# Performance work log

Hardware: AMD Instinct MI355X
Metric: run time of the kernel (lower is better)

The kernel has to match this reference:

```python
import jax, jax.numpy as jnp
import numpy as np

NH = 64
KS = 3
H_DIM = 32
IN_DIM = 1

# U-Net conv shapes, matching get_indices(unet_nh=64)
KERN_SHAPES = ([(NH, 2, KS, KS)] + [(NH, NH, KS, KS)] * 7
               + [(NH, 2 * NH, KS, KS), (NH, NH, KS, KS)] * 3
               + [(2, NH, 1, 1)])
BIAS_SHAPES = [(NH,)] * 14 + [(2,)]
KERN_SIZES = [int(np.prod(s)) for s in KERN_SHAPES]
BIAS_SIZES = [int(np.prod(s)) for s in BIAS_SHAPES]
OUT_DIM = sum(KERN_SIZES) + sum(BIAS_SIZES)  # 592002


def hypernet(hp, W1, b1, W2, b2, Wo, bo):
    # hp: [B, in_dim] -> per-sample flat weight vector [B, OUT_DIM]
    h = hp @ W1.T + b1          # no activation between lin1/lin2 (as in source)
    h = h @ W2.T + b2
    w = jnp.tanh(h @ Wo.T + bo)
    wl, bl = [], []
    off = 0
    for s, n in zip(KERN_SHAPES, KERN_SIZES):
        wl.append(w[:, off:off + n].reshape(-1, *s)); off += n
    for s, n in zip(BIAS_SHAPES, BIAS_SIZES):
        bl.append(w[:, off:off + n].reshape(-1, *s)); off += n
    return wl, bl, w


def bconv(x, w, b, pad):
    # per-sample conv: x [B,C,H,W], w [B,O,C,k,k], b [B,O]
    def one(xi, wi, bi):
        y = jax.lax.conv_general_dilated(xi[None], wi, (1, 1), [(pad, pad), (pad, pad)])
        return y[0] + bi[:, None, None]
    return jax.vmap(one)(x, w, b)


def maxpool2(x):
    B, C, H, W = x.shape
    return x.reshape(B, C, H // 2, 2, W // 2, 2).max(axis=(3, 5))


def up2_ac(x):
    # bilinear upsample scale=2, align_corners=True
    B, C, H, W = x.shape
    Ho, Wo = 2 * H, 2 * W
    ys = (jnp.arange(Ho, dtype=jnp.float32) * (H - 1) / (Ho - 1))
    y0 = jnp.floor(ys).astype(jnp.int32); y1 = jnp.minimum(y0 + 1, H - 1)
    wy = (ys - y0.astype(jnp.float32))[None, None, :, None]
    xs = (jnp.arange(Wo, dtype=jnp.float32) * (W - 1) / (Wo - 1))
    x0 = jnp.floor(xs).astype(jnp.int32); x1 = jnp.minimum(x0 + 1, W - 1)
    wx = (xs - x0.astype(jnp.float32))[None, None, None, :]
    r = x[:, :, y0, :] * (1 - wy) + x[:, :, y1, :] * wy
    return r[:, :, :, x0] * (1 - wx) + r[:, :, :, x1] * wx


def setup_inputs() -> dict:
    key = jax.random.key(0)
    ks = jax.random.split(key, 9)
    B, H, W = 8, 256, 256
    s1 = 1.0 / (IN_DIM * NH) ** 0.5
    s2 = 1.0 / (H_DIM * NH) ** 0.5
    return {
        "zf": jax.random.normal(ks[0], (B, H, W, 2), jnp.float32),
        "y": jax.random.normal(ks[1], (B, H, W, 2), jnp.float32),
        "hyperparams": jax.random.uniform(ks[2], (B, IN_DIM), jnp.float32),
        "W1": jax.random.normal(ks[3], (H_DIM, IN_DIM), jnp.float32) * s1,
        "b1": jax.random.normal(ks[4], (H_DIM,), jnp.float32) * s1,
        "W2": jax.random.normal(ks[5], (H_DIM, H_DIM), jnp.float32) * s2,
        "b2": jax.random.normal(ks[6], (H_DIM,), jnp.float32) * s2,
        "Wo": jax.random.normal(ks[7], (OUT_DIM, H_DIM), jnp.float32) * s2,
        "bo": jax.random.normal(ks[8], (OUT_DIM,), jnp.float32) * s2,
    }


def reference(zf, y, hyperparams, W1, b1, W2, b2, Wo, bo):
    wl, bl, flat = hypernet(hyperparams, W1, b1, W2, b2, Wo, bo)
    # l1 over all generated weights+biases == sum |flat| per sample
    l1_weights = jnp.sum(jnp.abs(flat), axis=1)
    relu = jax.nn.relu
    x = jnp.transpose(zf, (0, 3, 1, 2))  # [B,2,H,W]
    x = relu(bconv(x, wl[0], bl[0], 1))
    conv1 = relu(bconv(x, wl[1], bl[1], 1))
    x = maxpool2(conv1)
    x = relu(bconv(x, wl[2], bl[2], 1))
    conv2 = relu(bconv(x, wl[3], bl[3], 1))
    x = maxpool2(conv2)
    x = relu(bconv(x, wl[4], bl[4], 1))
    conv3 = relu(bconv(x, wl[5], bl[5], 1))
    x = maxpool2(conv3)
    x = relu(bconv(x, wl[6], bl[6], 1))
    conv4 = relu(bconv(x, wl[7], bl[7], 1))
    x = jnp.concatenate([up2_ac(conv4), conv3], axis=1)
    x = relu(bconv(x, wl[8], bl[8], 1))
    x = relu(bconv(x, wl[9], bl[9], 1))
    x = jnp.concatenate([up2_ac(x), conv2], axis=1)
    x = relu(bconv(x, wl[10], bl[10], 1))
    x = relu(bconv(x, wl[11], bl[11], 1))
    x = jnp.concatenate([up2_ac(x), conv1], axis=1)
    x = relu(bconv(x, wl[12], bl[12], 1))
    x = relu(bconv(x, wl[13], bl[13], 1))
    x = bconv(x, wl[14], bl[14], 0)  # 1x1 conv, padding=0
    x = jnp.transpose(x, (0, 2, 3, 1))
    x = zf + x  # residual=True
    return (x, l1_weights)
```

## Files before the change

### kernel.cpp

```cpp
#include <hip/hip_runtime.h>
#include <hip/hip_bf16.h>
#include <math.h>

#define ODIM 592002L
#define WRB  589824L
#define NB 8

typedef __hip_bfloat16 bf16;
typedef __bf16  bf16x8 __attribute__((ext_vector_type(8)));
typedef float   f32x16 __attribute__((ext_vector_type(16)));
typedef short   s16x8  __attribute__((ext_vector_type(8)));

__device__ __forceinline__ float b2f(bf16 x) { return __bfloat162float(x); }
__device__ __forceinline__ bf16 f2b(float x) { return __float2bfloat16(x); }
__device__ __forceinline__ bf16x8 bzero() { return __builtin_bit_cast(bf16x8, (s16x8)0); }

__global__ __launch_bounds__(256) void hyper_h(
    const float* __restrict__ hp, const float* __restrict__ W1,
    const float* __restrict__ b1, const float* __restrict__ W2,
    const float* __restrict__ b2, float* __restrict__ h2out)
{
    __shared__ float h1[NB][32];
    int t = threadIdx.x;
    int b = t >> 5, i = t & 31;
    h1[b][i] = hp[b] * W1[i] + b1[i];
    __syncthreads();
    float acc = b2[i];
    #pragma unroll
    for (int j = 0; j < 32; ++j) acc += h1[b][j] * W2[i * 32 + j];
    h2out[b * 32 + i] = acc;
}

__global__ __launch_bounds__(256) void genw(
    const float* __restrict__ Wo, const float* __restrict__ bo,
    const float* __restrict__ h2, bf16* __restrict__ wfb,
    float* __restrict__ part)
{
    __shared__ float h2s[256];
    __shared__ float red[256];
    int t = threadIdx.x;
    h2s[t] = h2[t];
    __syncthreads();
    long o = (long)blockIdx.x * 256 + t;
    float absacc[NB];
    #pragma unroll
    for (int b = 0; b < NB; ++b) absacc[b] = 0.f;
    if (o < ODIM) {
        float row[32];
        const float4* wp = (const float4*)(Wo + o * 32);
        #pragma unroll
        for (int q = 0; q < 8; ++q) {
            float4 v = wp[q];
            row[q*4+0] = v.x; row[q*4+1] = v.y; row[q*4+2] = v.z; row[q*4+3] = v.w;
        }
        float bias = bo[o];
        #pragma unroll
        for (int b = 0; b < NB; ++b) {
            float acc = bias;
            #pragma unroll
            for (int k = 0; k < 32; ++k) acc += h2s[b*32+k] * row[k];
            float w = tanhf(acc);
            wfb[(long)b * ODIM + o] = f2b(w);
            absacc[b] = fabsf(w);
        }
    }
    for (int b = 0; b < NB; ++b) {
        red[t] = absacc[b];
        __syncthreads();
        for (int s = 128; s > 0; s >>= 1) {
            if (t < s) red[t] += red[t + s];
            __syncthreads();
        }
        if (t == 0) part[(long)blockIdx.x * NB + b] = red[0];
        __syncthreads();
    }
}

__global__ __launch_bounds__(256) void l1_reduce(
    const float* __restrict__ part, int nblk, float* __restrict__ outp)
{
    __shared__ float red[256];
    int t = threadIdx.x; int b = t & 7, ch = t >> 3;
    float s = 0.f;
    for (int i = ch; i < nblk; i += 32) s += part[(long)i * 8 + b];
    red[t] = s;
    __syncthreads();
    for (int st = 128; st >= 8; st >>= 1) {
        if (t < st) red[t] += red[t + st];
        __syncthreads();
    }
    if (t < 8) outp[t] = red[t];
}

__global__ __launch_bounds__(256) void repack_all(
    const bf16* __restrict__ wfb, bf16* __restrict__ wr)
{
    int i = blockIdx.x * 256 + threadIdx.x;
    int b = blockIdx.y;
    if (i >= (int)WRB) return;
    int roff, koff, dual = 0;
    if      (i < 36864)  { roff = 0;      koff = 1152;  }
    else if (i < 73728)  { roff = 36864;  koff = 38016; }
    else if (i < 110592) { roff = 73728;  koff = 74880; }
    else if (i < 147456) { roff = 110592; koff = 111744;}
    else if (i < 184320) { roff = 147456; koff = 148608;}
    else if (i < 221184) { roff = 184320; koff = 185472;}
    else if (i < 258048) { roff = 221184; koff = 222336;}
    else if (i < 331776) { roff = 258048; koff = 259200; dual = 1; }
    else if (i < 368640) { roff = 331776; koff = 332928;}
    else if (i < 442368) { roff = 368640; koff = 369792; dual = 1; }
    else if (i < 479232) { roff = 442368; koff = 443520;}
    else if (i < 552960) { roff = 479232; koff = 480384; dual = 1; }
    else                 { roff = 552960; koff = 554112;}
    int li = i - roff;
    int Cinfull = dual ? 128 : 64;
    int fid = li >> 9;
    int lane = (li >> 3) & 63;
    int j = li & 7;
    int h = fid & 1;
    int kk = fid >> 1;
    int k4 = kk & 3;
    int tapq = kk >> 2;
    int tap = tapq % 9;
    int pass = tapq / 9;
    int oc = h * 32 + (lane & 31);
    int icf = pass * 64 + k4 * 16 + (lane >> 5) * 8 + j;
    wr[(long)b * WRB + i] =
        wfb[(long)b * ODIM + koff + ((long)oc * Cinfull + icf) * 9 + tap];
}

template<int TR, int TC, int MODE>
__device__ __forceinline__ void stage_tile(
    const bf16* __restrict__ src, int Hc, int Wc, int y0, int x0,
    bf16* lin, int t)
{
    const int XL = TC + 2;
    const int total = (TR + 2) * XL * 8;
    for (int idx = t; idx < total; idx += 256) {
        const int g = idx & 7;
        const int rem = idx >> 3;
        const int xl = rem % XL;
        const int gy = y0 + rem / XL - 1, gx = x0 + xl - 1;
        bf16x8 v = bzero();
        if ((unsigned)gy < (unsigned)Hc && (unsigned)gx < (unsigned)Wc) {
            if constexpr (MODE == 0) {
                v = *(const bf16x8*)(src + (((long)gy * Wc) + gx) * 64 + g * 8);
            } else if constexpr (MODE == 1) {
                const int Ws = Wc * 2;
                const bf16* p = src + (((long)(gy*2) * Ws) + gx*2) * 64 + g * 8;
                bf16x8 aa = *(const bf16x8*)p;
                bf16x8 bb = *(const bf16x8*)(p + 64);
                bf16x8 cc = *(const bf16x8*)(p + (long)Ws * 64);
                bf16x8 dd = *(const bf16x8*)(p + (long)Ws * 64 + 64);
                #pragma unroll
                for (int j = 0; j < 8; ++j) {
                    float m = fmaxf(fmaxf((float)aa[j], (float)bb[j]),
                                    fmaxf((float)cc[j], (float)dd[j]));
                    v[j] = (__bf16)m;
                }
            } else {
                const int Hs = Hc >> 1, Ws = Wc >> 1;
                const float sy = (float)(Hs - 1) / (float)(Hc - 1);
                const float sx = (float)(Ws - 1) / (float)(Wc - 1);
                float ys = gy * sy, xs = gx * sx;
                int yy0 = (int)ys, xx0 = (int)xs;
                int yy1 = min(yy0 + 1, Hs - 1), xx1 = min(xx0 + 1, Ws - 1);
                float wy = ys - (float)yy0, wx = xs - (float)xx0;
                bf16x8 q00 = *(const bf16x8*)(src + ((long)yy0*Ws + xx0)*64 + g*8);
                bf16x8 q01 = *(const bf16x8*)(src + ((long)yy0*Ws + xx1)*64 + g*8);
                bf16x8 q10 = *(const bf16x8*)(src + ((long)yy1*Ws + xx0)*64 + g*8);
                bf16x8 q11 = *(const bf16x8*)(src + ((long)yy1*Ws + xx1)*64 + g*8);
                #pragma unroll
                for (int j = 0; j < 8; ++j) {
                    float r0 = (float)q00[j]*(1.f-wx) + (float)q01[j]*wx;
                    float r1 = (float)q10[j]*(1.f-wx) + (float)q11[j]*wx;
                    v[j] = (__bf16)(r0*(1.f-wy) + r1*wy);
                }
            }
        }
        long byte = (((long)rem) * 128 + g * 16) ^ ((xl & 7) << 4);
        *(bf16x8*)((char*)lin + byte) = v;
    }
}

template<int MODE>
__global__ __launch_bounds__(256, 4) void conv_mfma(
    const bf16* __restrict__ src1, const bf16* __restrict__ src2,
    int Hc, int Wc,
    const bf16* __restrict__ wr, long roff,
    const bf16* __restrict__ wfb, int boff,
    bf16* __restrict__ outp)
{
    const int TR = 4, TC = 32, XL = TC + 2;
    __shared__ bf16 lin[(TR + 2) * XL * 64];
    __shared__ float biasf[64];
    const int t = threadIdx.x;
    const int lane = t & 63;
    const int w = t >> 6;
    const int half = w & 1;
    const int wrow = (w >> 1) * 2;
    const int b = blockIdx.z;
    const int y0 = blockIdx.y * TR;
    const int x0 = blockIdx.x * TC;
    const int lx = lane & 31;

    f32x16 acc0 = {}, acc1 = {};

    const bf16* wl = wr + (long)b * WRB + roff;
    if (t < 64) biasf[t] = b2f(wfb[(long)b * ODIM + boff + t]);

    const int icbl = (lane >> 5) * 16;

    auto kpass = [&](int p) {
        #pragma unroll
        for (int k4 = 0; k4 < 4; ++k4) {
            #pragma unroll
            for (int dxi = 0; dxi < 3; ++dxi) {
                const int xl = lx + dxi;
                const int co = xl * 128 + ((k4 * 32 + icbl) ^ ((xl & 7) << 4));
                bf16x8 bfr[4];
                #pragma unroll
                for (int rr = 0; rr < 4; ++rr)
                    bfr[rr] = *(const bf16x8*)((const char*)lin + (wrow + rr) * (XL * 128) + co);
                #pragma unroll
                for (int dy = 0; dy < 3; ++dy) {
                    const int fid = ((p * 9 + dy * 3 + dxi) * 4 + k4) * 2 + half;
                    bf16x8 a0 = *(const bf16x8*)(wl + ((long)fid << 9) + (lane << 3));
                    acc0 = __builtin_amdgcn_mfma_f32_32x32x16_bf16(a0, bfr[dy + 0], acc0, 0, 0, 0);
                    acc1 = __builtin_amdgcn_mfma_f32_32x32x16_bf16(a0, bfr[dy + 1], acc1, 0, 0, 0);
                }
            }
        }
    };

    stage_tile<TR, TC, MODE>(src1, Hc, Wc, y0, x0, lin, t);
    __syncthreads();
    kpass(0);
    if (src2) {
        __syncthreads();
        stage_tile<TR, TC, 0>(src2, Hc, Wc, y0, x0, lin, t);
        __syncthreads();
        kpass(1);
    }

    __syncthreads();
    #pragma unroll
    for (int r = 0; r < 2; ++r) {
        const int pixidx = (wrow + r) * TC + lx;
        const int psw = (pixidx & 7) << 4;
        const f32x16& A = r ? acc1 : acc0;
        #pragma unroll
        for (int q = 0; q < 4; ++q) {
            const int oc0 = half * 32 + 8 * q + 4 * (lane >> 5);
            ushort4 pk;
            float v0 = fmaxf(A[4*q+0] + biasf[oc0 + 0], 0.f);
            float v1 = fmaxf(A[4*q+1] + biasf[oc0 + 1], 0.f);
            float v2 = fmaxf(A[4*q+2] + biasf[oc0 + 2], 0.f);
            float v3 = fmaxf(A[4*q+3] + biasf[oc0 + 3], 0.f);
            pk.x = __builtin_bit_cast(unsigned short, f2b(v0));
            pk.y = __builtin_bit_cast(unsigned short, f2b(v1));
            pk.z = __builtin_bit_cast(unsigned short, f2b(v2));
            pk.w = __builtin_bit_cast(unsigned short, f2b(v3));
            long byte = ((long)pixidx * 128 + oc0 * 2) ^ psw;
            *(ushort4*)((char*)lin + byte) = pk;
        }
    }
    __syncthreads();
    bf16* outt = outp + (((long)b * Hc + y0) * Wc + x0) * 64;
    #pragma unroll
    for (int off = t * 16; off < TR * TC * 128; off += 4096) {
        int pix = off >> 7;
        int r = pix >> 5, c = pix & 31;
        long sb = (long)off ^ ((pix & 7) << 4);
        bf16x8 v = *(const bf16x8*)((const char*)lin + sb);
        *(bf16x8*)((char*)outt + ((long)(r * Wc + c)) * 128 + (off & 127)) = v;
    }
}

__global__ __launch_bounds__(256) void conv0_k(
    const float* __restrict__ zf, const bf16* __restrict__ wfb,
    bf16* __restrict__ outp)
{
    __shared__ float wsh[2][9][64];
    __shared__ float bsh[64];
    const int t = threadIdx.x;
    const int b = blockIdx.z;
    const long wb = (long)b * ODIM;
    for (int i = t; i < 1152; i += 256) {
        int oc = i / 18, r2 = i % 18, ic = r2 / 9, tap = r2 % 9;
        wsh[ic][tap][oc] = b2f(wfb[wb + i]);
    }
    if (t < 64) bsh[t] = b2f(wfb[wb + 591104 + t]);
    __syncthreads();
    const int pl = t >> 3, g = t & 7;
    const int pix = blockIdx.x * 32 + pl;
    const int y = pix >> 8, x = pix & 255;
    float acc[8];
    #pragma unroll
    for (int j = 0; j < 8; ++j) acc[j] = bsh[g * 8 + j];
    const float* zb = zf + (long)b * 131072;
    #pragma unroll
    for (int dy = 0; dy < 3; ++dy) {
        int yy = y + dy - 1;
        if ((unsigned)yy >= 256u) continue;
        #pragma unroll
        for (int dx = 0; dx < 3; ++dx) {
            int xx = x + dx - 1;
            if ((unsigned)xx >= 256u) continue;
            const float* p = zb + ((long)yy * 256 + xx) * 2;
            float v0 = p[0], v1 = p[1];
            int tap = dy * 3 + dx;
            #pragma unroll
            for (int j = 0; j < 8; ++j)
                acc[j] += v0 * wsh[0][tap][g*8+j] + v1 * wsh[1][tap][g*8+j];
        }
    }
    bf16x8 v;
    #pragma unroll
    for (int j = 0; j < 8; ++j) v[j] = (__bf16)fmaxf(acc[j], 0.f);
    *(bf16x8*)(outp + ((long)b * 65536 + pix) * 64 + g * 8) = v;
}

__global__ __launch_bounds__(256) void final_k(
    const bf16* __restrict__ X, const bf16* __restrict__ wfb,
    const float* __restrict__ zf, float* __restrict__ outp)
{
    __shared__ float wsh[128];
    __shared__ float bsh[2];
    const int t = threadIdx.x;
    const int i = blockIdx.x * 256 + t;
    const int pix = i & 65535;
    const int b = i >> 16;
    const long wb = (long)b * ODIM;
    if (t < 128) wsh[t] = b2f(wfb[wb + 590976 + t]);
    if (t < 2) bsh[t] = b2f(wfb[wb + 592000 + t]);
    __syncthreads();
    const bf16* p = X + ((long)b * 65536 + pix) * 64;
    float a0 = bsh[0], a1 = bsh[1];
    #pragma unroll
    for (int gq = 0; gq < 8; ++gq) {
        bf16x8 v = *(const bf16x8*)(p + gq * 8);
        #pragma unroll
        for (int j = 0; j < 8; ++j) {
            float f = (float)v[j];
            a0 += f * wsh[gq*8 + j];
            a1 += f * wsh[64 + gq*8 + j];
        }
    }
    long zi = ((long)b * 65536 + pix) * 2;
    outp[zi] = zf[zi] + a0;
    outp[zi + 1] = zf[zi + 1] + a1;
}

extern "C" void kernel_launch(void* const* d_in, const int* in_sizes, int n_in,
                              void* d_out, int out_size, void* d_ws, size_t ws_size,
                              hipStream_t stream)
{
    (void)in_sizes; (void)n_in; (void)out_size; (void)ws_size;
    const float* zf = (const float*)d_in[0];
    const float* hp = (const float*)d_in[2];
    const float* W1 = (const float*)d_in[3];
    const float* b1 = (const float*)d_in[4];
    const float* W2 = (const float*)d_in[5];
    const float* b2 = (const float*)d_in[6];
    const float* Wo = (const float*)d_in[7];
    const float* bo = (const float*)d_in[8];
    float* out = (float*)d_out;

    char* base = (char*)d_ws;
    float* h2   = (float*)base;  base += 1024;
    float* part = (float*)base;  base += 18504L * 4 + 32;
    bf16* wfb   = (bf16*)base;   base += 4736016L * 2 + 32;
    bf16* WREP  = (bf16*)base;   base += 4718592L * 2;
    bf16* Y256  = (bf16*)base;   base += 33554432L * 2;
    bf16* C1s   = (bf16*)base;   base += 33554432L * 2;
    bf16* D128a = (bf16*)base;   base += 8388608L * 2;
    bf16* C2s   = (bf16*)base;   base += 8388608L * 2;
    bf16* X128  = (bf16*)base;   base += 8388608L * 2;
    bf16* E64a  = (bf16*)base;   base += 2097152L * 2;
    bf16* C3s   = (bf16*)base;   base += 2097152L * 2;
    bf16* X64   = (bf16*)base;   base += 2097152L * 2;
    bf16* F32a  = (bf16*)base;   base += 524288L * 2;
    bf16* C4    = (bf16*)base;   base += 524288L * 2;

    hyper_h<<<1, 256, 0, stream>>>(hp, W1, b1, W2, b2, h2);
    const int ngb = (int)((ODIM + 255) / 256);
    genw<<<ngb, 256, 0, stream>>>(Wo, bo, h2, wfb, part);
    l1_reduce<<<1, 256, 0, stream>>>(part, ngb, out + 1048576);

    const int BB = 591104;
    const long R1=0, R2=36864, R3=73728, R4=110592, R5=147456, R6=184320,
               R7=221184, R8=258048, R9=331776, R10=368640, R11=442368,
               R12=479232, R13=552960;

    repack_all<<<dim3(2304, 8), 256, 0, stream>>>(wfb, WREP);

    conv0_k<<<dim3(2048, 1, 8), 256, 0, stream>>>(zf, wfb, Y256);

    conv_mfma<0><<<dim3(8,64,8),  256, 0, stream>>>(Y256, nullptr, 256,256, WREP, R1,  wfb, BB+64,  C1s);
    conv_mfma<1><<<dim3(4,32,8),  256, 0, stream>>>(C1s,  nullptr, 128,128, WREP, R2,  wfb, BB+128, D128a);
    conv_mfma<0><<<dim3(4,32,8),  256, 0, stream>>>(D128a,nullptr, 128,128, WREP, R3,  wfb, BB+192, C2s);
    conv_mfma<1><<<dim3(2,16,8),  256, 0, stream>>>(C2s,  nullptr, 64,64,   WREP, R4,  wfb, BB+256, E64a);
    conv_mfma<0><<<dim3(2,16,8),  256, 0, stream>>>(E64a, nullptr, 64,64,   WREP, R5,  wfb, BB+320, C3s);
    conv_mfma<1><<<dim3(1,8,8),   256, 0, stream>>>(C3s,  nullptr, 32,32,   WREP, R6,  wfb, BB+384, F32a);
    conv_mfma<0><<<dim3(1,8,8),   256, 0, stream>>>(F32a, nullptr, 32,32,   WREP, R7,  wfb, BB+448, C4);
    conv_mfma<2><<<dim3(2,16,8),  256, 0, stream>>>(C4,   C3s, 64,64,   WREP, R8,  wfb, BB+512, E64a);
    conv_mfma<0><<<dim3(2,16,8),  256, 0, stream>>>(E64a, nullptr, 64,64, WREP, R9,  wfb, BB+576, X64);
    conv_mfma<2><<<dim3(4,32,8),  256, 0, stream>>>(X64,  C2s, 128,128, WREP, R10, wfb, BB+640, D128a);
    conv_mfma<0><<<dim3(4,32,8),  256, 0, stream>>>(D128a,nullptr,128,128, WREP, R11, wfb, BB+704, X128);
    conv_mfma<2><<<dim3(8,64,8),  256, 0, stream>>>(X128, C1s, 256,256, WREP, R12, wfb, BB+768, Y256);
    conv_mfma<0><<<dim3(8,64,8),  256, 0, stream>>>(Y256, nullptr,256,256, WREP, R13, wfb, BB+832, C1s);

    final_k<<<dim3(2048), 256, 0, stream>>>(C1s, wfb, zf, out);
}
```

Measured before the change: 523.3 us.

## Read conv inputs directly from global memory for interior tiles, skip LDS staging

For interior tiles in plain-load mode, the conv kernel now loads input fragments straight from global memory into MFMA operands instead of staging the halo tile through LDS with barriers. Border tiles keep the LDS path, which now skips bounds checks when the tile is interior. The hypernet output also replaces tanhf with a fast exp/divide formulation. The direct path issues redundant global loads per wave that rely on cache hits, and it changes the memory access pattern.

```diff
diff --git a/kernel.cpp b/kernel.cpp
--- a/kernel.cpp
+++ b/kernel.cpp
@@ -59,9 +59,11 @@
             float acc = bias;
             #pragma unroll
             for (int k = 0; k < 32; ++k) acc += h2s[b*32+k] * row[k];
-            float w = tanhf(acc);
+            float e = __expf(-2.f * fabsf(acc));
+            float r = __fdividef(1.f - e, 1.f + e);
+            float w = (acc < 0.f) ? -r : r;
             wfb[(long)b * ODIM + o] = f2b(w);
-            absacc[b] = fabsf(w);
+            absacc[b] = r;
         }
     }
     for (int b = 0; b < NB; ++b) {
@@ -132,7 +134,7 @@
 template<int TR, int TC, int MODE>
 __device__ __forceinline__ void stage_tile(
     const bf16* __restrict__ src, int Hc, int Wc, int y0, int x0,
-    bf16* lin, int t)
+    bf16* lin, int t, bool interior)
 {
     const int XL = TC + 2;
     const int total = (TR + 2) * XL * 8;
@@ -142,7 +144,7 @@
         const int xl = rem % XL;
         const int gy = y0 + rem / XL - 1, gx = x0 + xl - 1;
         bf16x8 v = bzero();
-        if ((unsigned)gy < (unsigned)Hc && (unsigned)gx < (unsigned)Wc) {
+        if (interior || ((unsigned)gy < (unsigned)Hc && (unsigned)gx < (unsigned)Wc)) {
             if constexpr (MODE == 0) {
                 v = *(const bf16x8*)(src + (((long)gy * Wc) + gx) * 64 + g * 8);
             } else if constexpr (MODE == 1) {
@@ -203,6 +205,8 @@
     const int y0 = blockIdx.y * TR;
     const int x0 = blockIdx.x * TC;
     const int lx = lane & 31;
+    const bool interior = (y0 >= 1) & (y0 + TR + 1 <= Hc)
+                        & (x0 >= 1) & (x0 + TC + 1 <= Wc);
 
     f32x16 acc0 = {}, acc1 = {};
 
@@ -211,7 +215,7 @@
 
     const int icbl = (lane >> 5) * 16;
 
-    auto kpass = [&](int p) {
+    auto kpass_lds = [&](int p) {
         #pragma unroll
         for (int k4 = 0; k4 < 4; ++k4) {
             #pragma unroll
@@ -233,14 +237,59 @@
         }
     };
 
-    stage_tile<TR, TC, MODE>(src1, Hc, Wc, y0, x0, lin, t);
-    __syncthreads();
-    kpass(0);
+    auto kpass_dir = [&](const bf16* src, int p) {
+        const bf16* r0 = src + (((long)(y0 + wrow - 1) * Wc) + (x0 + lx - 1)) * 64 + (lane >> 5) * 8;
+        const long rs = (long)Wc * 64;
+        const bf16* r1 = r0 + rs;
+        const bf16* r2 = r1 + rs;
+        const bf16* r3 = r2 + rs;
+        #pragma unroll 1
+        for (int k4 = 0; k4 < 4; ++k4) {
+            #pragma unroll
+            for (int dxi = 0; dxi < 3; ++dxi) {
+                const int eo = dxi * 64 + k4 * 16;
+                bf16x8 b0 = *(const bf16x8*)(r0 + eo);
+                bf16x8 b1 = *(const bf16x8*)(r1 + eo);
+                bf16x8 b2v = *(const bf16x8*)(r2 + eo);
+                bf16x8 b3 = *(const bf16x8*)(r3 + eo);
+                {
+                    const int fid = ((p * 9 + 0 * 3 + dxi) * 4 + k4) * 2 + half;
+                    bf16x8 a0 = *(const bf16x8*)(wl + ((long)fid << 9) + (lane << 3));
+                    acc0 = __builtin_amdgcn_mfma_f32_32x32x16_bf16(a0, b0, acc0, 0, 0, 0);
+                    acc1 = __builtin_amdgcn_mfma_f32_32x32x16_bf16(a0, b1, acc1, 0, 0, 0);
+                }
+                {
+                    const int fid = ((p * 9 + 1 * 3 + dxi) * 4 + k4) * 2 + half;
+                    bf16x8 a0 = *(const bf16x8*)(wl + ((long)fid << 9) + (lane << 3));
+                    acc0 = __builtin_amdgcn_mfma_f32_32x32x16_bf16(a0, b1, acc0, 0, 0, 0);
+                    acc1 = __builtin_amdgcn_mfma_f32_32x32x16_bf16(a0, b2v, acc1, 0, 0, 0);
+                }
+                {
+                    const int fid = ((p * 9 + 2 * 3 + dxi) * 4 + k4) * 2 + half;
+                    bf16x8 a0 = *(const bf16x8*)(wl + ((long)fid << 9) + (lane << 3));
+                    acc0 = __builtin_amdgcn_mfma_f32_32x32x16_bf16(a0, b2v, acc0, 0, 0, 0);
+                    acc1 = __builtin_amdgcn_mfma_f32_32x32x16_bf16(a0, b3, acc1, 0, 0, 0);
+                }
+            }
+        }
+    };
+
+    if (MODE == 0 && interior) {
+        kpass_dir(src1, 0);
+    } else {
+        stage_tile<TR, TC, MODE>(src1, Hc, Wc, y0, x0, lin, t, interior);
+        __syncthreads();
+        kpass_lds(0);
+    }
     if (src2) {
-        __syncthreads();
-        stage_tile<TR, TC, 0>(src2, Hc, Wc, y0, x0, lin, t);
-        __syncthreads();
-        kpass(1);
+        if (interior) {
+            kpass_dir(src2, 1);
+        } else {
+            __syncthreads();
+            stage_tile<TR, TC, 0>(src2, Hc, Wc, y0, x0, lin, t, interior);
+            __syncthreads();
+            kpass_lds(1);
+        }
     }
 
     __syncthreads();
```

Result: slower. 733.4 us (+40.1%).
